# Performance work log

Hardware: AMD Instinct MI355X
Metric: run time of the kernel (lower is better)

Reference implementation:

```python
import jax, jax.numpy as jnp
import numpy as np

TEMPERATURE = 8.0  # sqrt(d_k) with d_k=64

def setup_inputs() -> dict:
    key = jax.random.key(0)
    k1, k2, k3, k4 = jax.random.split(key, 4)
    B, L, D = 64, 1024, 64  # B = batch*n_heads
    q = jax.random.normal(k1, (B, L, D), dtype=jnp.float32)
    k = jax.random.normal(k2, (B, L, D), dtype=jnp.float32)
    v = jax.random.normal(k3, (B, L, D), dtype=jnp.float32)
    mask = jax.random.randint(k4, (B, L, L), 0, 2).astype(jnp.bool_)
    return {"q": q, "k": k, "v": v, "mask": mask}

def reference(q, k, v, mask):
    # scores: [B, Lq, Lk]
    attn = jnp.einsum('bqd,bkd->bqk', q, k) / TEMPERATURE
    attn = jnp.where(mask, -jnp.inf, attn)
    attn = jax.nn.softmax(attn, axis=2)
    output = jnp.einsum('bqk,bkd->bqd', attn, v)
    return (output, attn)
```

## Files before the change

### kernel.cpp

```cpp
#include <hip/hip_runtime.h>

#define B_ 64
#define L_ 1024
#define D_ 64
#define QT 16

typedef _Float16 f16;
typedef __attribute__((ext_vector_type(8))) _Float16 f16x8;
typedef __attribute__((ext_vector_type(4))) float f32x4;

__device__ __forceinline__ int sidx(int row, int col) {
    return row * 1024 + ((((col >> 3) ^ (row & 7)) << 3) | (col & 7));
}

__global__ __launch_bounds__(256, 4)
void sdpa_kernel(const float* __restrict__ q, const float* __restrict__ kk,
                 const float* __restrict__ v, const unsigned char* __restrict__ mask,
                 float* __restrict__ out, float* __restrict__ attn)
{
    __shared__ f16 S[QT * 1024];
    __shared__ float wmax[4][QT];
    __shared__ float wsum[QT];

    const int tid = threadIdx.x;
    const int l = tid & 63, w = tid >> 6;
    const int lr = l & 15, lg = l >> 4;
    const int bid = blockIdx.x;
    const int b = bid >> 6, qt = bid & 63;
    const int qbase = b * L_ + qt * QT;

    unsigned det = 0;
    {
        const unsigned* mw = (const unsigned*)mask;
        #pragma unroll
        for (int i = 0; i < 32; ++i) det |= mw[i];
    }
    const bool elem4 = (det <= 1u) || (det == 0x3F800000u);

    f16x8 aqh[2], aql[2];
    {
        const float* qp = q + (size_t)(qbase + lr) * D_;
        #pragma unroll
        for (int s = 0; s < 2; ++s) {
            float4 f0 = *(const float4*)(qp + s * 32 + lg * 8);
            float4 f1 = *(const float4*)(qp + s * 32 + lg * 8 + 4);
            float fv[8] = {f0.x, f0.y, f0.z, f0.w, f1.x, f1.y, f1.z, f1.w};
            #pragma unroll
            for (int j = 0; j < 8; ++j) {
                f16 h = (f16)fv[j];
                aqh[s][j] = h;
                aql[s][j] = (f16)(fv[j] - (float)h);
            }
        }
    }

    float vmax[4] = {-INFINITY, -INFINITY, -INFINITY, -INFINITY};
    const float* kb = kk + (size_t)(b * L_ + w * 16 + lr) * D_ + lg * 8;
    const size_t mrowbase = (size_t)(qbase + lg * 4) * L_ + w * 16 + lr;

    float4 kc[4];
    kc[0] = *(const float4*)kb;
    kc[1] = *(const float4*)(kb + 4);
    kc[2] = *(const float4*)(kb + 32);
    kc[3] = *(const float4*)(kb + 36);
    int mcur[4], mnxt[4];
    #pragma unroll
    for (int r2 = 0; r2 < 4; ++r2) {
        if (elem4) {
            mcur[r2] = ((const int*)mask)[mrowbase + (size_t)r2 * L_];
            mnxt[r2] = ((const int*)mask)[mrowbase + (size_t)r2 * L_ + 64];
        } else {
            mcur[r2] = mask[mrowbase + (size_t)r2 * L_];
            mnxt[r2] = mask[mrowbase + (size_t)r2 * L_ + 64];
        }
    }

    for (int ck = 0; ck < 16; ++ck) {
        float4 kn[4];
        if (ck < 15) {
            const float* kp = kb + (size_t)(ck + 1) * 64 * D_;
            kn[0] = *(const float4*)kp;
            kn[1] = *(const float4*)(kp + 4);
            kn[2] = *(const float4*)(kp + 32);
            kn[3] = *(const float4*)(kp + 36);
        }
        int mfut[4];
        if (ck < 14) {
            const size_t mo = mrowbase + (size_t)(ck + 2) * 64;
            if (elem4) {
                #pragma unroll
                for (int r2 = 0; r2 < 4; ++r2) mfut[r2] = ((const int*)mask)[mo + (size_t)r2 * L_];
            } else {
                #pragma unroll
                for (int r2 = 0; r2 < 4; ++r2) mfut[r2] = mask[mo + (size_t)r2 * L_];
            }
        }
        f16x8 bh[2], bl[2];
        #pragma unroll
        for (int s = 0; s < 2; ++s) {
            float fv[8] = {kc[2*s].x, kc[2*s].y, kc[2*s].z, kc[2*s].w,
                           kc[2*s+1].x, kc[2*s+1].y, kc[2*s+1].z, kc[2*s+1].w};
            #pragma unroll
            for (int j = 0; j < 8; ++j) {
                f16 h = (f16)fv[j];
                bh[s][j] = h;
                bl[s][j] = (f16)(fv[j] - (float)h);
            }
        }
        f32x4 acc = {0.f, 0.f, 0.f, 0.f};
        #pragma unroll
        for (int s = 0; s < 2; ++s) {
            acc = __builtin_amdgcn_mfma_f32_16x16x32_f16(aqh[s], bh[s], acc, 0, 0, 0);
            acc = __builtin_amdgcn_mfma_f32_16x16x32_f16(aql[s], bh[s], acc, 0, 0, 0);
            acc = __builtin_amdgcn_mfma_f32_16x16x32_f16(aqh[s], bl[s], acc, 0, 0, 0);
        }
        const int scol = ck * 64 + w * 16 + lr;
        #pragma unroll
        for (int r2 = 0; r2 < 4; ++r2) {
            float sv = mcur[r2] ? -INFINITY : acc[r2] * 0.125f;
            S[sidx(lg * 4 + r2, scol)] = (f16)sv;
            vmax[r2] = fmaxf(vmax[r2], sv);
        }
        #pragma unroll
        for (int r2 = 0; r2 < 4; ++r2) { mcur[r2] = mnxt[r2]; }
        if (ck < 14) {
            #pragma unroll
            for (int r2 = 0; r2 < 4; ++r2) { mnxt[r2] = mfut[r2]; }
        }
        if (ck < 15) {
            #pragma unroll
            for (int j = 0; j < 4; ++j) kc[j] = kn[j];
        }
    }
    #pragma unroll
    for (int r2 = 0; r2 < 4; ++r2) {
        #pragma unroll
        for (int off = 1; off < 16; off <<= 1)
            vmax[r2] = fmaxf(vmax[r2], __shfl_xor(vmax[r2], off));
    }
    if (lr == 0) {
        #pragma unroll
        for (int r2 = 0; r2 < 4; ++r2) wmax[w][lg * 4 + r2] = vmax[r2];
    }
    __syncthreads();

    {
        const int row = tid >> 4, cg = tid & 15;
        const float m = fmaxf(fmaxf(wmax[0][row], wmax[1][row]),
                              fmaxf(wmax[2][row], wmax[3][row]));
        float sum = 0.f;
        #pragma unroll
        for (int c = 0; c < 8; ++c) {
            f16* sp = &S[row * 1024 + ((((cg + 16 * c)) ^ (row & 7)) << 3)];
            f16x8 sv = *(const f16x8*)sp;
            f16x8 ev;
            #pragma unroll
            for (int j = 0; j < 8; ++j) {
                float e = __expf((float)sv[j] - m);
                ev[j] = (f16)e;
                sum += e;
            }
            *(f16x8*)sp = ev;
        }
        #pragma unroll
        for (int off = 1; off < 16; off <<= 1) sum += __shfl_xor(sum, off);
        if (cg == 0) wsum[row] = sum;
        __syncthreads();

        const float inv = 1.0f / wsum[row];
        float* ap = attn + (size_t)(qbase + row) * L_;
        #pragma unroll
        for (int c = 0; c < 8; ++c) {
            f16x8 ev = *(const f16x8*)&S[row * 1024 + (((cg + 16 * c) ^ (row & 7)) << 3)];
            float4 p0, p1;
            p0.x = (float)ev[0] * inv; p0.y = (float)ev[1] * inv;
            p0.z = (float)ev[2] * inv; p0.w = (float)ev[3] * inv;
            p1.x = (float)ev[4] * inv; p1.y = (float)ev[5] * inv;
            p1.z = (float)ev[6] * inv; p1.w = (float)ev[7] * inv;
            *(float4*)(ap + (cg + 16 * c) * 8)     = p0;
            *(float4*)(ap + (cg + 16 * c) * 8 + 4) = p1;
        }
    }

    f32x4 acc2 = {0.f, 0.f, 0.f, 0.f};
    const float* vb = v + (size_t)(b * L_) * D_ + w * 16 + lr;
    float vcA[8], vcB[8];
    #pragma unroll
    for (int j = 0; j < 8; ++j) {
        vcA[j] = vb[(size_t)(lg * 8 + j) * D_];
        vcB[j] = vb[(size_t)(32 + lg * 8 + j) * D_];
    }
    for (int tt = 0; tt < 16; ++tt) {
        {
            f16x8 pa = *(const f16x8*)&S[lr * 1024 + ((((2 * tt) * 4 + lg) ^ (lr & 7)) << 3)];
            f16x8 bv;
            #pragma unroll
            for (int j = 0; j < 8; ++j) bv[j] = (f16)vcA[j];
            if (tt < 15) {
                const float* vp = vb + (size_t)((2 * tt + 2) * 32 + lg * 8) * D_;
                #pragma unroll
                for (int j = 0; j < 8; ++j) vcA[j] = vp[(size_t)j * D_];
            }
            acc2 = __builtin_amdgcn_mfma_f32_16x16x32_f16(pa, bv, acc2, 0, 0, 0);
        }
        {
            f16x8 pa = *(const f16x8*)&S[lr * 1024 + ((((2 * tt + 1) * 4 + lg) ^ (lr & 7)) << 3)];
            f16x8 bv;
            #pragma unroll
            for (int j = 0; j < 8; ++j) bv[j] = (f16)vcB[j];
            if (tt < 15) {
                const float* vp = vb + (size_t)((2 * tt + 3) * 32 + lg * 8) * D_;
                #pragma unroll
                for (int j = 0; j < 8; ++j) vcB[j] = vp[(size_t)j * D_];
            }
            acc2 = __builtin_amdgcn_mfma_f32_16x16x32_f16(pa, bv, acc2, 0, 0, 0);
        }
    }

    #pragma unroll
    for (int r2 = 0; r2 < 4; ++r2) {
        const float invr = 1.0f / wsum[lg * 4 + r2];
        out[(size_t)(qbase + lg * 4 + r2) * D_ + w * 16 + lr] = acc2[r2] * invr;
    }
}

extern "C" void kernel_launch(void* const* d_in, const int* in_sizes, int n_in,
                              void* d_out, int out_size, void* d_ws, size_t ws_size,
                              hipStream_t stream) {
    const float* q = (const float*)d_in[0];
    const float* k = (const float*)d_in[1];
    const float* v = (const float*)d_in[2];
    const unsigned char* mask = (const unsigned char*)d_in[3];
    float* out = (float*)d_out;
    float* attn = out + (size_t)B_ * L_ * D_;
    dim3 grid(B_ * (L_ / QT));
    sdpa_kernel<<<grid, 256, 0, stream>>>(q, k, v, mask, out, attn);
}
```

Baseline: 302.9 us.

## Precompute fp16 split K, transposed fp16 V, and bit-packed mask in workspace prepasses

Adds three prepass kernels. One converts K to pre-scaled hi/lo fp16 pairs, one transposes V to fp16, and one packs the mask into bitmasks. The main kernel then reads compact operands instead of redoing conversions and re-reading the full byte/int mask in each of the 64 query-tile blocks per batch. The output and attention stores become nontemporal. This cuts redundant global traffic and ALU work in the main kernel, at the cost of extra launches and a full pass over the mask. It falls back to the original kernel if the workspace is too small.

Result: slower. 337.5 us (+11.4%).

```diff
diff --git a/kernel.cpp b/kernel.cpp
--- a/kernel.cpp
+++ b/kernel.cpp
@@ -9,14 +9,246 @@
 typedef __attribute__((ext_vector_type(8))) _Float16 f16x8;
 typedef __attribute__((ext_vector_type(4))) float f32x4;
 
+#define WS_KH 0u
+#define WS_KL 8388608u
+#define WS_VT 16777216u
+#define WS_BM 25165824u
+#define WS_NEED 33554432u
+
 __device__ __forceinline__ int sidx(int row, int col) {
     return row * 1024 + ((((col >> 3) ^ (row & 7)) << 3) | (col & 7));
 }
 
+
+__global__ __launch_bounds__(256)
+void prep_k(const float* __restrict__ kk, f16* __restrict__ kh, f16* __restrict__ kl) {
+    const int i = (blockIdx.x * 256 + threadIdx.x) * 8;
+    float4 f0 = *(const float4*)(kk + i);
+    float4 f1 = *(const float4*)(kk + i + 4);
+    float fv[8] = {f0.x, f0.y, f0.z, f0.w, f1.x, f1.y, f1.z, f1.w};
+    f16x8 h, lo;
+    #pragma unroll
+    for (int j = 0; j < 8; ++j) {
+        float x = fv[j] * 0.125f;
+        f16 hh = (f16)x;
+        h[j] = hh;
+        lo[j] = (f16)(x - (float)hh);
+    }
+    *(f16x8*)(kh + i) = h;
+    *(f16x8*)(kl + i) = lo;
+}
+
+__global__ __launch_bounds__(256)
+void prep_v(const float* __restrict__ v, f16* __restrict__ vt) {
+    __shared__ f16 tile[64][72];
+    const int b = blockIdx.x >> 4, kt = blockIdx.x & 15;
+    const int r = threadIdx.x >> 2, c0 = (threadIdx.x & 3) * 16;
+    const float* vp = v + (size_t)(b * L_ + kt * 64 + r) * D_ + c0;
+    float4 g0 = *(const float4*)vp;
+    float4 g1 = *(const float4*)(vp + 4);
+    float4 g2 = *(const float4*)(vp + 8);
+    float4 g3 = *(const float4*)(vp + 12);
+    float fv[16] = {g0.x, g0.y, g0.z, g0.w, g1.x, g1.y, g1.z, g1.w,
+                    g2.x, g2.y, g2.z, g2.w, g3.x, g3.y, g3.z, g3.w};
+    #pragma unroll
+    for (int j = 0; j < 16; ++j) tile[r][c0 + j] = (f16)fv[j];
+    __syncthreads();
+    f16x8 o0, o1;
+    #pragma unroll
+    for (int j = 0; j < 8; ++j) { o0[j] = tile[c0 + j][r]; o1[j] = tile[c0 + 8 + j][r]; }
+    f16* op = vt + (size_t)(b * 64 + r) * 1024 + kt * 64 + c0;
+    *(f16x8*)op = o0;
+    *(f16x8*)(op + 8) = o1;
+}
+
+__global__ __launch_bounds__(256)
+void prep_mask(const unsigned char* __restrict__ mask, unsigned* __restrict__ bits) {
+    unsigned det = 0;
+    {
+        const unsigned* mw = (const unsigned*)mask;
+        #pragma unroll
+        for (int i = 0; i < 32; ++i) det |= mw[i];
+    }
+    const bool elem4 = (det <= 1u) || (det == 0x3F800000u);
+    const size_t total = (size_t)B_ * L_ * L_;
+    const size_t stride = (size_t)gridDim.x * blockDim.x;
+    const int lane = threadIdx.x & 63;
+    for (size_t idx = (size_t)blockIdx.x * blockDim.x + threadIdx.x; idx < total; idx += stride) {
+        int val = elem4 ? ((const int*)mask)[idx] : (int)mask[idx];
+        unsigned long long bal = __ballot(val != 0);
+        if (lane == 0)       bits[idx >> 5] = (unsigned)bal;
+        else if (lane == 32) bits[idx >> 5] = (unsigned)(bal >> 32);
+    }
+}
+
+
 __global__ __launch_bounds__(256, 4)
-void sdpa_kernel(const float* __restrict__ q, const float* __restrict__ kk,
-                 const float* __restrict__ v, const unsigned char* __restrict__ mask,
-                 float* __restrict__ out, float* __restrict__ attn)
+void sdpa_main(const float* __restrict__ q, const f16* __restrict__ kh,
+               const f16* __restrict__ kl, const f16* __restrict__ vt,
+               const unsigned* __restrict__ bits,
+               float* __restrict__ out, float* __restrict__ attn)
+{
+    __shared__ f16 S[QT * 1024];
+    __shared__ float wmax[4][QT];
+    __shared__ float wsum[QT];
+
+    const int tid = threadIdx.x;
+    const int l = tid & 63, w = tid >> 6;
+    const int lr = l & 15, lg = l >> 4;
+    const int bid = blockIdx.x;
+    const int b = bid >> 6, qt = bid & 63;
+    const int qbase = b * L_ + qt * QT;
+
+    f16x8 aqh[2], aql[2];
+    {
+        const float* qp = q + (size_t)(qbase + lr) * D_;
+        #pragma unroll
+        for (int s = 0; s < 2; ++s) {
+            float4 f0 = *(const float4*)(qp + s * 32 + lg * 8);
+            float4 f1 = *(const float4*)(qp + s * 32 + lg * 8 + 4);
+            float fv[8] = {f0.x, f0.y, f0.z, f0.w, f1.x, f1.y, f1.z, f1.w};
+            #pragma unroll
+            for (int j = 0; j < 8; ++j) {
+                f16 h = (f16)fv[j];
+                aqh[s][j] = h;
+                aql[s][j] = (f16)(fv[j] - (float)h);
+            }
+        }
+    }
+
+    const f16* khp = kh + (size_t)(b * L_ + w * 16 + lr) * D_ + lg * 8;
+    const f16* klp = kl + (size_t)(b * L_ + w * 16 + lr) * D_ + lg * 8;
+    const unsigned* bmp = bits + (size_t)(qbase + lg * 4) * 32 + ((w * 16 + lr) >> 5);
+    const int bitpos = (w * 16 + lr) & 31;
+
+    f16x8 bhc[2], blc[2];
+    bhc[0] = *(const f16x8*)khp;        bhc[1] = *(const f16x8*)(khp + 32);
+    blc[0] = *(const f16x8*)klp;        blc[1] = *(const f16x8*)(klp + 32);
+    unsigned mcur[4], mnxt[4];
+    #pragma unroll
+    for (int r2 = 0; r2 < 4; ++r2) { mcur[r2] = bmp[r2 * 32]; mnxt[r2] = bmp[r2 * 32 + 2]; }
+
+    float vmax[4] = {-INFINITY, -INFINITY, -INFINITY, -INFINITY};
+    for (int ck = 0; ck < 16; ++ck) {
+        f16x8 bhn[2], bln[2];
+        if (ck < 15) {
+            const f16* p1 = khp + (size_t)(ck + 1) * 64 * D_;
+            const f16* p2 = klp + (size_t)(ck + 1) * 64 * D_;
+            bhn[0] = *(const f16x8*)p1; bhn[1] = *(const f16x8*)(p1 + 32);
+            bln[0] = *(const f16x8*)p2; bln[1] = *(const f16x8*)(p2 + 32);
+        }
+        unsigned mfut[4];
+        if (ck < 14) {
+            #pragma unroll
+            for (int r2 = 0; r2 < 4; ++r2) mfut[r2] = bmp[r2 * 32 + (ck + 2) * 2];
+        }
+        f32x4 acc = {0.f, 0.f, 0.f, 0.f};
+        #pragma unroll
+        for (int s = 0; s < 2; ++s) {
+            acc = __builtin_amdgcn_mfma_f32_16x16x32_f16(aqh[s], bhc[s], acc, 0, 0, 0);
+            acc = __builtin_amdgcn_mfma_f32_16x16x32_f16(aql[s], bhc[s], acc, 0, 0, 0);
+            acc = __builtin_amdgcn_mfma_f32_16x16x32_f16(aqh[s], blc[s], acc, 0, 0, 0);
+        }
+        const int scol = ck * 64 + w * 16 + lr;
+        #pragma unroll
+        for (int r2 = 0; r2 < 4; ++r2) {
+            float sv = ((mcur[r2] >> bitpos) & 1u) ? -INFINITY : acc[r2];
+            S[sidx(lg * 4 + r2, scol)] = (f16)sv;
+            vmax[r2] = fmaxf(vmax[r2], sv);
+        }
+        #pragma unroll
+        for (int r2 = 0; r2 < 4; ++r2) mcur[r2] = mnxt[r2];
+        if (ck < 14) {
+            #pragma unroll
+            for (int r2 = 0; r2 < 4; ++r2) mnxt[r2] = mfut[r2];
+        }
+        if (ck < 15) {
+            #pragma unroll
+            for (int s = 0; s < 2; ++s) { bhc[s] = bhn[s]; blc[s] = bln[s]; }
+        }
+    }
+    #pragma unroll
+    for (int r2 = 0; r2 < 4; ++r2) {
+        #pragma unroll
+        for (int off = 1; off < 16; off <<= 1)
+            vmax[r2] = fmaxf(vmax[r2], __shfl_xor(vmax[r2], off));
+    }
+    if (lr == 0) {
+        #pragma unroll
+        for (int r2 = 0; r2 < 4; ++r2) wmax[w][lg * 4 + r2] = vmax[r2];
+    }
+    __syncthreads();
+
+    {
+        const int row = tid >> 4, cg = tid & 15;
+        const float m = fmaxf(fmaxf(wmax[0][row], wmax[1][row]),
+                              fmaxf(wmax[2][row], wmax[3][row]));
+        float sum = 0.f;
+        #pragma unroll
+        for (int c = 0; c < 8; ++c) {
+            f16* sp = &S[row * 1024 + (((cg + 16 * c) ^ (row & 7)) << 3)];
+            f16x8 sv = *(const f16x8*)sp;
+            f16x8 ev;
+            #pragma unroll
+            for (int j = 0; j < 8; ++j) {
+                float e = __expf((float)sv[j] - m);
+                ev[j] = (f16)e;
+                sum += e;
+            }
+            *(f16x8*)sp = ev;
+        }
+        #pragma unroll
+        for (int off = 1; off < 16; off <<= 1) sum += __shfl_xor(sum, off);
+        if (cg == 0) wsum[row] = sum;
+        __syncthreads();
+
+        const float inv = 1.0f / wsum[row];
+        float* ap = attn + (size_t)(qbase + row) * L_;
+        #pragma unroll
+        for (int c = 0; c < 8; ++c) {
+            f16x8 ev = *(const f16x8*)&S[row * 1024 + (((cg + 16 * c) ^ (row & 7)) << 3)];
+            f32x4 p0, p1;
+            p0[0] = (float)ev[0] * inv; p0[1] = (float)ev[1] * inv;
+            p0[2] = (float)ev[2] * inv; p0[3] = (float)ev[3] * inv;
+            p1[0] = (float)ev[4] * inv; p1[1] = (float)ev[5] * inv;
+            p1[2] = (float)ev[6] * inv; p1[3] = (float)ev[7] * inv;
+            __builtin_nontemporal_store(p0, (f32x4*)(ap + (cg + 16 * c) * 8));
+            __builtin_nontemporal_store(p1, (f32x4*)(ap + (cg + 16 * c) * 8 + 4));
+        }
+    }
+
+    f32x4 acc2 = {0.f, 0.f, 0.f, 0.f};
+    const f16* vtp = vt + (size_t)(b * 64 + w * 16 + lr) * 1024 + lg * 8;
+    f16x8 vA = *(const f16x8*)vtp;
+    f16x8 vB = *(const f16x8*)(vtp + 32);
+    for (int tt = 0; tt < 16; ++tt) {
+        {
+            f16x8 pa = *(const f16x8*)&S[lr * 1024 + ((((2 * tt) * 4 + lg) ^ (lr & 7)) << 3)];
+            f16x8 bv = vA;
+            if (tt < 15) vA = *(const f16x8*)(vtp + (2 * tt + 2) * 32);
+            acc2 = __builtin_amdgcn_mfma_f32_16x16x32_f16(pa, bv, acc2, 0, 0, 0);
+        }
+        {
+            f16x8 pa = *(const f16x8*)&S[lr * 1024 + ((((2 * tt + 1) * 4 + lg) ^ (lr & 7)) << 3)];
+            f16x8 bv = vB;
+            if (tt < 15) vB = *(const f16x8*)(vtp + (2 * tt + 3) * 32);
+            acc2 = __builtin_amdgcn_mfma_f32_16x16x32_f16(pa, bv, acc2, 0, 0, 0);
+        }
+    }
+
+    #pragma unroll
+    for (int r2 = 0; r2 < 4; ++r2) {
+        const float invr = 1.0f / wsum[lg * 4 + r2];
+        __builtin_nontemporal_store(acc2[r2] * invr,
+            out + (size_t)(qbase + lg * 4 + r2) * D_ + w * 16 + lr);
+    }
+}
+
+
+__global__ __launch_bounds__(256, 4)
+void sdpa_fallback(const float* __restrict__ q, const float* __restrict__ kk,
+                   const float* __restrict__ v, const unsigned char* __restrict__ mask,
+                   float* __restrict__ out, float* __restrict__ attn)
 {
     __shared__ f16 S[QT * 1024];
     __shared__ float wmax[4][QT];
@@ -122,10 +354,10 @@
             vmax[r2] = fmaxf(vmax[r2], sv);
         }
         #pragma unroll
-        for (int r2 = 0; r2 < 4; ++r2) { mcur[r2] = mnxt[r2]; }
+        for (int r2 = 0; r2 < 4; ++r2) mcur[r2] = mnxt[r2];
         if (ck < 14) {
             #pragma unroll
-            for (int r2 = 0; r2 < 4; ++r2) { mnxt[r2] = mfut[r2]; }
+            for (int r2 = 0; r2 < 4; ++r2) mnxt[r2] = mfut[r2];
         }
         if (ck < 15) {
             #pragma unroll
@@ -151,7 +383,7 @@
         float sum = 0.f;
         #pragma unroll
         for (int c = 0; c < 8; ++c) {
-            f16* sp = &S[row * 1024 + ((((cg + 16 * c)) ^ (row & 7)) << 3)];
+            f16* sp = &S[row * 1024 + (((cg + 16 * c) ^ (row & 7)) << 3)];
             f16x8 sv = *(const f16x8*)sp;
             f16x8 ev;
             #pragma unroll
@@ -233,6 +465,17 @@
     const unsigned char* mask = (const unsigned char*)d_in[3];
     float* out = (float*)d_out;
     float* attn = out + (size_t)B_ * L_ * D_;
-    dim3 grid(B_ * (L_ / QT));
-    sdpa_kernel<<<grid, 256, 0, stream>>>(q, k, v, mask, out, attn);
-}
+
+    if (ws_size >= (size_t)WS_NEED) {
+        f16* kh = (f16*)((char*)d_ws + WS_KH);
+        f16* kl = (f16*)((char*)d_ws + WS_KL);
+        f16* vt = (f16*)((char*)d_ws + WS_VT);
+        unsigned* bits = (unsigned*)((char*)d_ws + WS_BM);
+        prep_k<<<dim3(2048), 256, 0, stream>>>(k, kh, kl);
+        prep_v<<<dim3(1024), 256, 0, stream>>>(v, vt);
+        prep_mask<<<dim3(4096), 256, 0, stream>>>(mask, bits);
+        sdpa_main<<<dim3(B_ * (L_ / QT)), 256, 0, stream>>>(q, kh, kl, vt, bits, out, attn);
+    } else {
+        sdpa_fallback<<<dim3(B_ * (L_ / QT)), 256, 0, stream>>>(q, k, v, mask, out, attn);
+    }
+}
```

## Precompute fp16 K, transposed V and packed mask bits; two-pass softmax without LDS

Applied to the files above, without the earlier changes.

Adds a prep kernel that converts K to pre-scaled fp16, transposes V to fp16, and packs the boolean mask into bitmasks in workspace. The main kernel gives each wave one 16-row query tile. It recomputes QK^T twice: first to get the row sum of exp, then to write normalized probabilities and accumulate PV with MFMA. This removes LDS score storage and the max reduction and cuts mask traffic in the main pass. In exchange it drops the split-precision QK, skips max-subtraction (safe only for bounded scores), and adds an extra launch and recompute.

Result: slower. 328.9 us (+8.6%).

```diff
diff --git a/kernel.cpp b/kernel.cpp
--- a/kernel.cpp
+++ b/kernel.cpp
@@ -7,16 +7,217 @@
 
 typedef _Float16 f16;
 typedef __attribute__((ext_vector_type(8))) _Float16 f16x8;
+typedef __attribute__((ext_vector_type(4))) _Float16 f16x4;
 typedef __attribute__((ext_vector_type(4))) float f32x4;
+typedef unsigned long long u64;
+typedef unsigned long long u64x4 __attribute__((ext_vector_type(4)));
+
+#define WS_KH 0u
+#define WS_VT 8388608u
+#define WS_BT 16777216u
+#define WS_NEED 25165824u
+
+#define MFMA32(A, B, C) __builtin_amdgcn_mfma_f32_16x16x32_f16((A), (B), (C), 0, 0, 0)
+#define PV16(A, B, C)   __builtin_amdgcn_mfma_f32_16x16x16f16((A), (B), (C), 0, 0, 0)
+
+__global__ __launch_bounds__(256)
+void mega_prep(const float* __restrict__ kk, const float* __restrict__ v,
+               const unsigned char* __restrict__ mask,
+               f16* __restrict__ kh, f16* __restrict__ vt, u64* __restrict__ bits) {
+    __shared__ f16 tile[64][72];
+    const int bid = blockIdx.x;
+    if (bid < 2048) {
+        const int i = (bid * 256 + threadIdx.x) * 8;
+        float4 f0 = *(const float4*)(kk + i);
+        float4 f1 = *(const float4*)(kk + i + 4);
+        float fv[8] = {f0.x, f0.y, f0.z, f0.w, f1.x, f1.y, f1.z, f1.w};
+        f16x8 h;
+        #pragma unroll
+        for (int j = 0; j < 8; ++j) h[j] = (f16)(fv[j] * 0.125f);
+        *(f16x8*)(kh + i) = h;
+    } else if (bid < 3072) {
+        const int bb = bid - 2048;
+        const int b = bb >> 4, kt = bb & 15;
+        const int r = threadIdx.x >> 2, c0 = (threadIdx.x & 3) * 16;
+        const float* vp = v + (size_t)(b * L_ + kt * 64 + r) * D_ + c0;
+        float4 g0 = *(const float4*)vp;
+        float4 g1 = *(const float4*)(vp + 4);
+        float4 g2 = *(const float4*)(vp + 8);
+        float4 g3 = *(const float4*)(vp + 12);
+        float fv[16] = {g0.x, g0.y, g0.z, g0.w, g1.x, g1.y, g1.z, g1.w,
+                        g2.x, g2.y, g2.z, g2.w, g3.x, g3.y, g3.z, g3.w};
+        #pragma unroll
+        for (int j = 0; j < 16; ++j) tile[r][c0 + j] = (f16)fv[j];
+        __syncthreads();
+        f16x8 o0, o1;
+        #pragma unroll
+        for (int j = 0; j < 8; ++j) { o0[j] = tile[c0 + j][r]; o1[j] = tile[c0 + 8 + j][r]; }
+        f16* op = vt + (size_t)(b * 64 + r) * 1024 + kt * 64 + c0;
+        *(f16x8*)op = o0;
+        *(f16x8*)(op + 8) = o1;
+    } else {
+        unsigned det = 0;
+        {
+            const unsigned* mw = (const unsigned*)mask;
+            #pragma unroll
+            for (int i = 0; i < 32; ++i) det |= mw[i];
+        }
+        const bool elem4 = (det <= 1u) || (det == 0x3F800000u);
+        const int lane = threadIdx.x & 63;
+        const int gw = (bid - 3072) * 4 + (threadIdx.x >> 6);
+        for (int s = gw; s < 262144; s += 8192) {
+            unsigned nib;
+            if (elem4) {
+                const int4 m = *(const int4*)((const int*)mask + (size_t)s * 256 + lane * 4);
+                nib = (m.x != 0 ? 1u : 0u) | (m.y != 0 ? 2u : 0u) |
+                      (m.z != 0 ? 4u : 0u) | (m.w != 0 ? 8u : 0u);
+            } else {
+                const uchar4 m = *(const uchar4*)(mask + (size_t)s * 256 + lane * 4);
+                nib = (m.x ? 1u : 0u) | (m.y ? 2u : 0u) | (m.z ? 4u : 0u) | (m.w ? 8u : 0u);
+            }
+            u64 b0 = __ballot((nib & 1u) != 0u);
+            u64 b1 = __ballot((nib & 2u) != 0u);
+            u64 b2 = __ballot((nib & 4u) != 0u);
+            u64 b3 = __ballot((nib & 8u) != 0u);
+            if (lane == 0) {
+                u64x4 o = {b0, b1, b2, b3};
+                *(u64x4*)(bits + (size_t)s * 4) = o;
+            }
+        }
+    }
+}
+
+
+__global__ __launch_bounds__(256, 4)
+void sdpa_main(const float* __restrict__ q, const f16* __restrict__ kh,
+               const f16* __restrict__ vt, const u64* __restrict__ bits,
+               float* __restrict__ out, float* __restrict__ attn)
+{
+    const int tid = threadIdx.x;
+    const int l = tid & 63, w = tid >> 6;
+    const int lr = l & 15, lg = l >> 4;
+    const int bid0 = blockIdx.x;
+    const int bid = (bid0 & 7) * 128 + (bid0 >> 3);
+    const int tile_id = bid * 4 + w;
+    const int b = tile_id >> 6;
+    const int qbase = tile_id * QT;
+
+    f16x8 aq0, aq1;
+    {
+        const float* qp = q + (size_t)(qbase + lr) * D_;
+        float4 f0 = *(const float4*)(qp + lg * 8);
+        float4 f1 = *(const float4*)(qp + lg * 8 + 4);
+        float4 f2 = *(const float4*)(qp + 32 + lg * 8);
+        float4 f3 = *(const float4*)(qp + 32 + lg * 8 + 4);
+        aq0[0] = (f16)f0.x; aq0[1] = (f16)f0.y; aq0[2] = (f16)f0.z; aq0[3] = (f16)f0.w;
+        aq0[4] = (f16)f1.x; aq0[5] = (f16)f1.y; aq0[6] = (f16)f1.z; aq0[7] = (f16)f1.w;
+        aq1[0] = (f16)f2.x; aq1[1] = (f16)f2.y; aq1[2] = (f16)f2.z; aq1[3] = (f16)f2.w;
+        aq1[4] = (f16)f3.x; aq1[5] = (f16)f3.y; aq1[6] = (f16)f3.z; aq1[7] = (f16)f3.w;
+    }
+
+    const f16* khb = kh + (size_t)b * (L_ * D_) + lg * 8;
+    const f16* vtb = vt + (size_t)b * (D_ * L_);
+    const u64x4* bp = (const u64x4*)bits + (size_t)(qbase + lr) * 4;
+
+    float rsum = 0.f;
+    f16x8 kc0, kc1;
+    {
+        const f16* kp = khb + (size_t)lr * D_;
+        kc0 = *(const f16x8*)kp;
+        kc1 = *(const f16x8*)(kp + 32);
+    }
+    #pragma unroll
+    for (int sp = 0; sp < 4; ++sp) {
+        const u64x4 bw = bp[sp];
+        #pragma unroll 4
+        for (int cc = 0; cc < 16; ++cc) {
+            const int c = sp * 16 + cc;
+            f16x8 kn0, kn1;
+            if (c < 63) {
+                const f16* kp = khb + (size_t)((c + 1) * 16 + lr) * D_;
+                kn0 = *(const f16x8*)kp;
+                kn1 = *(const f16x8*)(kp + 32);
+            }
+            f32x4 s = {0.f, 0.f, 0.f, 0.f};
+            s = MFMA32(kc0, aq0, s);
+            s = MFMA32(kc1, aq1, s);
+            const int sh = cc * 4 + lg;
+            rsum += ((unsigned)(bw[0] >> sh) & 1u) ? 0.f : __expf(s[0]);
+            rsum += ((unsigned)(bw[1] >> sh) & 1u) ? 0.f : __expf(s[1]);
+            rsum += ((unsigned)(bw[2] >> sh) & 1u) ? 0.f : __expf(s[2]);
+            rsum += ((unsigned)(bw[3] >> sh) & 1u) ? 0.f : __expf(s[3]);
+            kc0 = kn0; kc1 = kn1;
+        }
+    }
+    rsum += __shfl_xor(rsum, 16);
+    rsum += __shfl_xor(rsum, 32);
+    const float inv = 1.0f / rsum;
+
+    f32x4 o0 = {0.f,0.f,0.f,0.f}, o1 = {0.f,0.f,0.f,0.f};
+    f32x4 o2 = {0.f,0.f,0.f,0.f}, o3 = {0.f,0.f,0.f,0.f};
+    {
+        const f16* kp = khb + (size_t)lr * D_;
+        kc0 = *(const f16x8*)kp;
+        kc1 = *(const f16x8*)(kp + 32);
+    }
+    float* ap = attn + (size_t)(qbase + lr) * L_ + lg * 4;
+    const f16* vpb = vtb + (size_t)lr * L_ + lg * 4;
+    #pragma unroll
+    for (int sp = 0; sp < 4; ++sp) {
+        const u64x4 bw = bp[sp];
+        #pragma unroll 4
+        for (int cc = 0; cc < 16; ++cc) {
+            const int c = sp * 16 + cc;
+            f16x8 kn0, kn1;
+            if (c < 63) {
+                const f16* kp = khb + (size_t)((c + 1) * 16 + lr) * D_;
+                kn0 = *(const f16x8*)kp;
+                kn1 = *(const f16x8*)(kp + 32);
+            }
+            f32x4 s = {0.f, 0.f, 0.f, 0.f};
+            s = MFMA32(kc0, aq0, s);
+            s = MFMA32(kc1, aq1, s);
+            const int sh = cc * 4 + lg;
+            f32x4 p;
+            p[0] = (((unsigned)(bw[0] >> sh) & 1u) ? 0.f : __expf(s[0])) * inv;
+            p[1] = (((unsigned)(bw[1] >> sh) & 1u) ? 0.f : __expf(s[1])) * inv;
+            p[2] = (((unsigned)(bw[2] >> sh) & 1u) ? 0.f : __expf(s[2])) * inv;
+            p[3] = (((unsigned)(bw[3] >> sh) & 1u) ? 0.f : __expf(s[3])) * inv;
+            *(f32x4*)(ap + c * 16) = p;
+            f16x4 pa;
+            pa[0] = (f16)p[0]; pa[1] = (f16)p[1]; pa[2] = (f16)p[2]; pa[3] = (f16)p[3];
+            const f16* vp = vpb + c * 16;
+            f16x4 v0 = *(const f16x4*)vp;
+            f16x4 v1 = *(const f16x4*)(vp + 16 * L_);
+            f16x4 v2 = *(const f16x4*)(vp + 32 * L_);
+            f16x4 v3 = *(const f16x4*)(vp + 48 * L_);
+            o0 = PV16(pa, v0, o0);
+            o1 = PV16(pa, v1, o1);
+            o2 = PV16(pa, v2, o2);
+            o3 = PV16(pa, v3, o3);
+            kc0 = kn0; kc1 = kn1;
+        }
+    }
+
+    float* op = out + (size_t)(qbase + lg * 4) * D_ + lr;
+    #pragma unroll
+    for (int r = 0; r < 4; ++r) {
+        op[r * D_ + 0]  = o0[r];
+        op[r * D_ + 16] = o1[r];
+        op[r * D_ + 32] = o2[r];
+        op[r * D_ + 48] = o3[r];
+    }
+}
+
 
 __device__ __forceinline__ int sidx(int row, int col) {
     return row * 1024 + ((((col >> 3) ^ (row & 7)) << 3) | (col & 7));
 }
 
 __global__ __launch_bounds__(256, 4)
-void sdpa_kernel(const float* __restrict__ q, const float* __restrict__ kk,
-                 const float* __restrict__ v, const unsigned char* __restrict__ mask,
-                 float* __restrict__ out, float* __restrict__ attn)
+void sdpa_fallback(const float* __restrict__ q, const float* __restrict__ kk,
+                   const float* __restrict__ v, const unsigned char* __restrict__ mask,
+                   float* __restrict__ out, float* __restrict__ attn)
 {
     __shared__ f16 S[QT * 1024];
     __shared__ float wmax[4][QT];
@@ -110,9 +311,9 @@
         f32x4 acc = {0.f, 0.f, 0.f, 0.f};
         #pragma unroll
         for (int s = 0; s < 2; ++s) {
-            acc = __builtin_amdgcn_mfma_f32_16x16x32_f16(aqh[s], bh[s], acc, 0, 0, 0);
-            acc = __builtin_amdgcn_mfma_f32_16x16x32_f16(aql[s], bh[s], acc, 0, 0, 0);
-            acc = __builtin_amdgcn_mfma_f32_16x16x32_f16(aqh[s], bl[s], acc, 0, 0, 0);
+            acc = MFMA32(aqh[s], bh[s], acc);
+            acc = MFMA32(aql[s], bh[s], acc);
+            acc = MFMA32(aqh[s], bl[s], acc);
         }
         const int scol = ck * 64 + w * 16 + lr;
         #pragma unroll
@@ -122,10 +323,10 @@
             vmax[r2] = fmaxf(vmax[r2], sv);
         }
         #pragma unroll
-        for (int r2 = 0; r2 < 4; ++r2) { mcur[r2] = mnxt[r2]; }
+        for (int r2 = 0; r2 < 4; ++r2) mcur[r2] = mnxt[r2];
         if (ck < 14) {
             #pragma unroll
-            for (int r2 = 0; r2 < 4; ++r2) { mnxt[r2] = mfut[r2]; }
+            for (int r2 = 0; r2 < 4; ++r2) mnxt[r2] = mfut[r2];
         }
         if (ck < 15) {
             #pragma unroll
@@ -151,16 +352,16 @@
         float sum = 0.f;
         #pragma unroll
         for (int c = 0; c < 8; ++c) {
-            f16* sp = &S[row * 1024 + ((((cg + 16 * c)) ^ (row & 7)) << 3)];
+            f16* sp = &S[row * 1024 + (((cg + 16 * c) ^ (row & 7)) << 3)];
             f16x8 sv = *(const f16x8*)sp;
-            f16x8 ev;
+            f16x8 evv;
             #pragma unroll
             for (int j = 0; j < 8; ++j) {
                 float e = __expf((float)sv[j] - m);
-                ev[j] = (f16)e;
+                evv[j] = (f16)e;
                 sum += e;
             }
-            *(f16x8*)sp = ev;
+            *(f16x8*)sp = evv;
         }
         #pragma unroll
         for (int off = 1; off < 16; off <<= 1) sum += __shfl_xor(sum, off);
@@ -171,12 +372,12 @@
         float* ap = attn + (size_t)(qbase + row) * L_;
         #pragma unroll
         for (int c = 0; c < 8; ++c) {
-            f16x8 ev = *(const f16x8*)&S[row * 1024 + (((cg + 16 * c) ^ (row & 7)) << 3)];
+            f16x8 evv = *(const f16x8*)&S[row * 1024 + (((cg + 16 * c) ^ (row & 7)) << 3)];
             float4 p0, p1;
-            p0.x = (float)ev[0] * inv; p0.y = (float)ev[1] * inv;
-            p0.z = (float)ev[2] * inv; p0.w = (float)ev[3] * inv;
-            p1.x = (float)ev[4] * inv; p1.y = (float)ev[5] * inv;
-            p1.z = (float)ev[6] * inv; p1.w = (float)ev[7] * inv;
+            p0.x = (float)evv[0] * inv; p0.y = (float)evv[1] * inv;
+            p0.z = (float)evv[2] * inv; p0.w = (float)evv[3] * inv;
+            p1.x = (float)evv[4] * inv; p1.y = (float)evv[5] * inv;
+            p1.z = (float)evv[6] * inv; p1.w = (float)evv[7] * inv;
             *(float4*)(ap + (cg + 16 * c) * 8)     = p0;
             *(float4*)(ap + (cg + 16 * c) * 8 + 4) = p1;
         }
@@ -201,7 +402,7 @@
                 #pragma unroll
                 for (int j = 0; j < 8; ++j) vcA[j] = vp[(size_t)j * D_];
             }
-            acc2 = __builtin_amdgcn_mfma_f32_16x16x32_f16(pa, bv, acc2, 0, 0, 0);
+            acc2 = MFMA32(pa, bv, acc2);
         }
         {
             f16x8 pa = *(const f16x8*)&S[lr * 1024 + ((((2 * tt + 1) * 4 + lg) ^ (lr & 7)) << 3)];
@@ -213,7 +414,7 @@
                 #pragma unroll
                 for (int j = 0; j < 8; ++j) vcB[j] = vp[(size_t)j * D_];
             }
-            acc2 = __builtin_amdgcn_mfma_f32_16x16x32_f16(pa, bv, acc2, 0, 0, 0);
+            acc2 = MFMA32(pa, bv, acc2);
         }
     }
 
@@ -233,6 +434,14 @@
     const unsigned char* mask = (const unsigned char*)d_in[3];
     float* out = (float*)d_out;
     float* attn = out + (size_t)B_ * L_ * D_;
-    dim3 grid(B_ * (L_ / QT));
-    sdpa_kernel<<<grid, 256, 0, stream>>>(q, k, v, mask, out, attn);
+
+    if (ws_size >= (size_t)WS_NEED) {
+        f16* kh = (f16*)((char*)d_ws + WS_KH);
+        f16* vt = (f16*)((char*)d_ws + WS_VT);
+        u64* bits = (u64*)((char*)d_ws + WS_BT);
+        mega_prep<<<dim3(5120), 256, 0, stream>>>(k, v, mask, kh, vt, bits);
+        sdpa_main<<<dim3(1024), 256, 0, stream>>>(q, kh, vt, bits, out, attn);
+    } else {
+        sdpa_fallback<<<dim3(B_ * (L_ / QT)), 256, 0, stream>>>(q, k, v, mask, out, attn);
+    }
 }
```
